# Optimization experiments

Hardware: AMD Instinct MI355X
Metric: run time of the kernel (lower is better)

Reference implementation:

```python
import jax, jax.numpy as jnp
import numpy as np

B, S, D, H = 4, 2048, 768, 12
HD = D // H  # head_dim = 64


def setup_inputs() -> dict:
    key = jax.random.key(0)
    ks = jax.random.split(key, 5)
    scale = 0.02
    return {
        "x": jax.random.normal(ks[0], (B, S, D), dtype=jnp.float32),
        "wq": jax.random.normal(ks[1], (D, D), dtype=jnp.float32) * scale,
        "wk": jax.random.normal(ks[2], (D, D), dtype=jnp.float32) * scale,
        "wv": jax.random.normal(ks[3], (D, D), dtype=jnp.float32) * scale,
        "wo": jax.random.normal(ks[4], (D, D), dtype=jnp.float32) * scale,
        "bo": jnp.zeros((D,), dtype=jnp.float32),
    }


def reference(x, wq, wk, wv, wo, bo):
    b, s, d = x.shape
    # torch Linear: y = x @ W.T ; qkv_bias=False
    q = (x @ wq.T).reshape(b, s, H, HD).transpose(0, 2, 1, 3)  # [b,h,s,hd]
    k = (x @ wk.T).reshape(b, s, H, HD).transpose(0, 2, 1, 3)
    v = (x @ wv.T).reshape(b, s, H, HD).transpose(0, 2, 1, 3)
    scores = jnp.einsum("bhqd,bhkd->bhqk", q, k)  # full [b,h,s,s] score matrix
    causal = jnp.triu(jnp.ones((s, s), dtype=bool), k=1)
    scores = jnp.where(causal, -jnp.inf, scores)
    attn = jax.nn.softmax(scores / jnp.sqrt(jnp.float32(HD)), axis=-1)
    ctx = jnp.einsum("bhqk,bhkd->bhqd", attn, v)
    ctx = ctx.transpose(0, 2, 1, 3).reshape(b, s, d)
    return ctx @ wo.T + bo  # dropout is identity in eval mode
```

## Files before the change

### kernel.cpp

```cpp
#include <hip/hip_runtime.h>

#define H 12
#define S 2048
#define D 768
#define HD 64
#define BATCH 4
#define M_TOT (BATCH * S)

typedef __attribute__((ext_vector_type(8))) short bf16x8;
typedef __attribute__((ext_vector_type(4))) float f32x4;

__device__ __forceinline__ ushort f2bf(float f) {
  unsigned int x = __float_as_uint(f);
  x += 0x7fffu + ((x >> 16) & 1u);
  return (ushort)(x >> 16);
}

__device__ __forceinline__ uint cvt_pk_bf16(float lo, float hi) {
  uint r;
  asm("v_cvt_pk_bf16_f32 %0, %1, %2" : "=v"(r) : "v"(lo), "v"(hi));
  return r;
}

__device__ __forceinline__ void gload_lds16(const void* gsrc, void* lds) {
  __builtin_amdgcn_global_load_lds(
      (const __attribute__((address_space(1))) unsigned int*)gsrc,
      (__attribute__((address_space(3))) unsigned int*)lds, 16, 0, 0);
}

__global__ __launch_bounds__(256) void cast_all(
    const float* __restrict__ x, const float* __restrict__ wq,
    const float* __restrict__ wk, const float* __restrict__ wv,
    const float* __restrict__ wo, ushort* __restrict__ xb,
    ushort* __restrict__ wqb, ushort* __restrict__ wkb,
    ushort* __restrict__ wvb, ushort* __restrict__ wob) {
  const int NX = M_TOT * D / 4;
  const int NW = D * D / 4;
  int i = blockIdx.x * 256 + threadIdx.x;
  const float* src; ushort* dst; int off;
  if (i < NX) { src = x; dst = xb; off = i; }
  else {
    int j = i - NX; int w = j / NW; off = j - w * NW;
    src = (w == 0) ? wq : (w == 1) ? wk : (w == 2) ? wv : wo;
    dst = (w == 0) ? wqb : (w == 1) ? wkb : (w == 2) ? wvb : wob;
  }
  float4 f = reinterpret_cast<const float4*>(src)[off];
  ushort4 u;
  u.x = f2bf(f.x); u.y = f2bf(f.y); u.z = f2bf(f.z); u.w = f2bf(f.w);
  reinterpret_cast<ushort4*>(dst)[off] = u;
}

__global__ __launch_bounds__(256) void gemm128(const ushort* __restrict__ A,
                                               const ushort* __restrict__ W0,
                                               const ushort* __restrict__ W1,
                                               ushort* __restrict__ o0,
                                               ushort* __restrict__ o1,
                                               float* __restrict__ out_f,
                                               const float* __restrict__ bias,
                                               int mode, float oscale) {
  __shared__ ushort SM[2][8192];
  const int tid = threadIdx.x;
  const int lane = tid & 63, wid = tid >> 6;
  const int g = lane >> 4, li = lane & 15;
  const int wm = wid >> 1, wn = wid & 1;
  const int m0 = blockIdx.x * 128;
  const ushort* Wp = W0;
  ushort* ob = o0;
  float osc = oscale;
  int n0;
  if (mode == 0) {
    int y = blockIdx.y;
    if (y >= 6) { Wp = W1; ob = o1; osc = 1.0f; }
    n0 = (y % 6) * 128;
  } else {
    n0 = blockIdx.y * 128;
  }

  const int rsub = lane >> 2;
  const int coff = (((lane & 3) ^ ((rsub >> 1) & 3)) << 3);

  auto stage = [&](int buf, int k0) {
#pragma unroll
    for (int rnd = 0; rnd < 2; ++rnd) {
      const int row0 = rnd * 64 + wid * 16;
      gload_lds16(&A[(size_t)(m0 + row0 + rsub) * 768 + k0 + coff], &SM[buf][row0 * 32]);
      gload_lds16(&Wp[(size_t)(n0 + row0 + rsub) * 768 + k0 + coff],
                  &SM[buf][4096 + row0 * 32]);
    }
  };

  f32x4 acc[4][4] = {};
  stage(0, 0);

  for (int kt = 0; kt < 24; ++kt) {
    const int cur = kt & 1;
    asm volatile("s_waitcnt vmcnt(0)" ::: "memory");
    __syncthreads();
    if (kt + 1 < 24) stage(cur ^ 1, (kt + 1) * 32);

    bf16x8 a[4], b[4];
#pragma unroll
    for (int i = 0; i < 4; ++i) {
      const int row = wm * 64 + i * 16 + li;
      a[i] = *reinterpret_cast<const bf16x8*>(
          &SM[cur][row * 32 + ((g ^ ((row >> 1) & 3)) << 3)]);
    }
#pragma unroll
    for (int j = 0; j < 4; ++j) {
      const int row = wn * 64 + j * 16 + li;
      b[j] = *reinterpret_cast<const bf16x8*>(
          &SM[cur][4096 + row * 32 + ((g ^ ((row >> 1) & 3)) << 3)]);
    }
    __builtin_amdgcn_s_setprio(1);
#pragma unroll
    for (int i = 0; i < 4; ++i)
#pragma unroll
      for (int j = 0; j < 4; ++j)
        acc[i][j] = __builtin_amdgcn_mfma_f32_16x16x32_bf16(a[i], b[j], acc[i][j], 0, 0, 0);
    __builtin_amdgcn_s_setprio(0);
  }

  if (mode == 1) {
#pragma unroll
    for (int i = 0; i < 4; ++i)
#pragma unroll
      for (int j = 0; j < 4; ++j)
#pragma unroll
        for (int r = 0; r < 4; ++r) {
          const int m = m0 + wm * 64 + i * 16 + g * 4 + r;
          const int n = n0 + wn * 64 + j * 16 + li;
          out_f[(size_t)m * 768 + n] = acc[i][j][r] + bias[n];
        }
    return;
  }

  __syncthreads();
  ushort* Cs = &SM[0][0];
#pragma unroll
  for (int i = 0; i < 4; ++i)
#pragma unroll
    for (int j = 0; j < 4; ++j)
#pragma unroll
      for (int r = 0; r < 4; ++r) {
        const int row = wm * 64 + i * 16 + g * 4 + r;
        const int col = wn * 64 + j * 16 + li;
        const int pc = ((((col >> 3) ^ (row & 7)) << 3) | (col & 7));
        Cs[row * 128 + pc] = f2bf(acc[i][j][r] * osc);
      }
  __syncthreads();

  const int row = tid >> 1, half = tid & 1;
  ushort* dst;
  if (mode == 0) {
    const int m = m0 + row;
    const int b_ = m >> 11, s_ = m & 2047;
    const int h_ = (n0 >> 6) + half;
    dst = &ob[(((size_t)b_ * H + h_) * S + s_) * HD];
  } else {
    const int mf = m0 + row;
    const int b_ = n0 >> 11;
    const int h_ = mf >> 6, hd_ = mf & 63;
    dst = &ob[(((size_t)b_ * H + h_) * HD + hd_) * S + (n0 & 2047) + half * 64];
  }
#pragma unroll
  for (int c8 = 0; c8 < 8; ++c8) {
    const int col = half * 64 + c8 * 8;
    const int chunk = (col >> 3) ^ (row & 7);
    bf16x8 vv = *reinterpret_cast<const bf16x8*>(&Cs[row * 128 + chunk * 8]);
    *reinterpret_cast<bf16x8*>(&dst[c8 * 8]) = vv;
  }
}

__global__ __launch_bounds__(256) void attn_kernel(const ushort* __restrict__ Q,
                                                   const ushort* __restrict__ K,
                                                   const ushort* __restrict__ VT,
                                                   ushort* __restrict__ ctx) {
  __shared__ ushort Ks[2][64 * 64];
  __shared__ ushort Vts[2][64 * 64];
  __shared__ ushort Ps[4][32][72];

  const int tid = threadIdx.x;
  const int lane = tid & 63, wid = tid >> 6;
  const int g = lane >> 4, li = lane & 15;

  const int wg = blockIdx.x;
  const int xcd = wg & 7, t = wg >> 3;
  const int bh = xcd + 8 * (t >> 4);
  const int p = t & 15;
  const int qL = 64 * (31 - p);
  const int qS = 64 * p;

  const size_t base = (size_t)bh * S * HD;
  const size_t vtbase = (size_t)bh * HD * S;

  bf16x8 aq[2][2];
#pragma unroll
  for (int f = 0; f < 2; ++f) {
    const size_t qr = base + (size_t)((f ? qS : qL) + wid * 16 + li) * HD;
#pragma unroll
    for (int c = 0; c < 2; ++c)
      aq[f][c] = *reinterpret_cast<const bf16x8*>(&Q[qr + c * 32 + g * 8]);
  }

  f32x4 acc[2][4] = {};
  float lpart[2] = {0.f, 0.f};

  const int nkt = 32 - p;

  const int rsub = lane >> 3;
  const int c8e = (((lane & 7) ^ rsub) << 3);

  auto stage = [&](int buf, int k0) {
#pragma unroll
    for (int rnd = 0; rnd < 2; ++rnd) {
      const int row0 = rnd * 32 + wid * 8;
      gload_lds16(&K[base + (size_t)(k0 + row0 + rsub) * HD + c8e], &Ks[buf][row0 << 6]);
      gload_lds16(&VT[vtbase + (size_t)(row0 + rsub) * S + k0 + c8e], &Vts[buf][row0 << 6]);
    }
  };

  stage(0, 0);

  for (int kt = 0; kt < nkt; ++kt) {
    const int cur = kt & 1;
    const int k0 = kt * 64;
    const bool doS = (kt <= p);

    asm volatile("s_waitcnt vmcnt(0)" ::: "memory");
    __syncthreads();
    if (kt + 1 < nkt) stage(cur ^ 1, k0 + 64);

    f32x4 sc[2][4];
    __builtin_amdgcn_s_setprio(1);
#pragma unroll
    for (int ct = 0; ct < 4; ++ct) {
      const int row = ct * 16 + li, r7 = row & 7;
      const ushort* kr = &Ks[cur][row << 6];
      bf16x8 kb0 = *reinterpret_cast<const bf16x8*>(&kr[(g ^ r7) << 3]);
      bf16x8 kb1 = *reinterpret_cast<const bf16x8*>(&kr[((4 + g) ^ r7) << 3]);
      {
        f32x4 z = {};
        z = __builtin_amdgcn_mfma_f32_16x16x32_bf16(kb0, aq[0][0], z, 0, 0, 0);
        z = __builtin_amdgcn_mfma_f32_16x16x32_bf16(kb1, aq[0][1], z, 0, 0, 0);
        sc[0][ct] = z;
      }
      if (doS) {
        f32x4 z = {};
        z = __builtin_amdgcn_mfma_f32_16x16x32_bf16(kb0, aq[1][0], z, 0, 0, 0);
        z = __builtin_amdgcn_mfma_f32_16x16x32_bf16(kb1, aq[1][1], z, 0, 0, 0);
        sc[1][ct] = z;
      }
    }
    __builtin_amdgcn_s_setprio(0);

    if (kt == nkt - 1) {
      const int q = qL + wid * 16 + li;
#pragma unroll
      for (int ct = 0; ct < 4; ++ct)
#pragma unroll
        for (int r = 0; r < 4; ++r)
          if (k0 + ct * 16 + 4 * g + r > q) sc[0][ct][r] = -1e30f;
    }
    if (kt == p) {
      const int q = qS + wid * 16 + li;
#pragma unroll
      for (int ct = 0; ct < 4; ++ct)
#pragma unroll
        for (int r = 0; r < 4; ++r)
          if (k0 + ct * 16 + 4 * g + r > q) sc[1][ct][r] = -1e30f;
    }

#pragma unroll
    for (int f = 0; f < 2; ++f) {
      if (f == 1 && !doS) break;
#pragma unroll
      for (int ct = 0; ct < 4; ++ct) {
        float p0 = __builtin_amdgcn_exp2f(sc[f][ct][0]);
        float p1 = __builtin_amdgcn_exp2f(sc[f][ct][1]);
        float p2 = __builtin_amdgcn_exp2f(sc[f][ct][2]);
        float p3 = __builtin_amdgcn_exp2f(sc[f][ct][3]);
        lpart[f] += (p0 + p1) + (p2 + p3);
        uint2 pw;
        pw.x = cvt_pk_bf16(p0, p1);
        pw.y = cvt_pk_bf16(p2, p3);
        *reinterpret_cast<uint2*>(&Ps[wid][f * 16 + li][ct * 16 + 4 * g]) = pw;
      }
    }

    bf16x8 pa[2][2];
    pa[0][0] = *reinterpret_cast<const bf16x8*>(&Ps[wid][li][g * 8]);
    pa[0][1] = *reinterpret_cast<const bf16x8*>(&Ps[wid][li][32 + g * 8]);
    if (doS) {
      pa[1][0] = *reinterpret_cast<const bf16x8*>(&Ps[wid][16 + li][g * 8]);
      pa[1][1] = *reinterpret_cast<const bf16x8*>(&Ps[wid][16 + li][32 + g * 8]);
    }
    __builtin_amdgcn_s_setprio(1);
#pragma unroll
    for (int dt = 0; dt < 4; ++dt) {
      const int row = dt * 16 + li, r7 = row & 7;
      const ushort* vr = &Vts[cur][row << 6];
      bf16x8 vb0 = *reinterpret_cast<const bf16x8*>(&vr[(g ^ r7) << 3]);
      bf16x8 vb1 = *reinterpret_cast<const bf16x8*>(&vr[((4 + g) ^ r7) << 3]);
      acc[0][dt] = __builtin_amdgcn_mfma_f32_16x16x32_bf16(pa[0][0], vb0, acc[0][dt], 0, 0, 0);
      acc[0][dt] = __builtin_amdgcn_mfma_f32_16x16x32_bf16(pa[0][1], vb1, acc[0][dt], 0, 0, 0);
      if (doS) {
        acc[1][dt] = __builtin_amdgcn_mfma_f32_16x16x32_bf16(pa[1][0], vb0, acc[1][dt], 0, 0, 0);
        acc[1][dt] = __builtin_amdgcn_mfma_f32_16x16x32_bf16(pa[1][1], vb1, acc[1][dt], 0, 0, 0);
      }
    }
    __builtin_amdgcn_s_setprio(0);
  }

  const int b = bh / H, h = bh % H;
#pragma unroll
  for (int f = 0; f < 2; ++f) {
    float l = lpart[f];
    l += __shfl_xor(l, 16);
    l += __shfl_xor(l, 32);
#pragma unroll
    for (int r = 0; r < 4; ++r) {
      float inv = 1.0f / __shfl(l, 4 * g + r);
      const int s = (f ? qS : qL) + wid * 16 + 4 * g + r;
#pragma unroll
      for (int dt = 0; dt < 4; ++dt)
        ctx[((size_t)(b * S + s)) * D + h * HD + dt * 16 + li] =
            f2bf(acc[f][dt][r] * inv);
    }
  }
}

extern "C" void kernel_launch(void* const* d_in, const int* in_sizes, int n_in,
                              void* d_out, int out_size, void* d_ws, size_t ws_size,
                              hipStream_t stream) {
  (void)in_sizes; (void)n_in; (void)out_size; (void)ws_size;
  const float* x  = (const float*)d_in[0];
  const float* wq = (const float*)d_in[1];
  const float* wk = (const float*)d_in[2];
  const float* wv = (const float*)d_in[3];
  const float* wo = (const float*)d_in[4];
  const float* bo = (const float*)d_in[5];
  float* out = (float*)d_out;

  const size_t xn = (size_t)M_TOT * D;
  const size_t wn = (size_t)D * D;

  ushort* p = (ushort*)d_ws;
  ushort* x_bf  = p; p += xn;
  ushort* wq_bf = p; p += wn;
  ushort* wk_bf = p; p += wn;
  ushort* wv_bf = p; p += wn;
  ushort* wo_bf = p; p += wn;
  ushort* q_bf  = p; p += xn;
  ushort* k_bf  = p; p += xn;
  ushort* vt_bf = p; p += xn;
  ushort* ctx_bf = x_bf;

  cast_all<<<8448, 256, 0, stream>>>(x, wq, wk, wv, wo,
                                     x_bf, wq_bf, wk_bf, wv_bf, wo_bf);

  const float QSCALE = 0.125f * 1.44269504f;
  gemm128<<<dim3(64, 12), 256, 0, stream>>>(x_bf, wq_bf, wk_bf, q_bf, k_bf,
                                            nullptr, nullptr, 0, QSCALE);
  gemm128<<<dim3(6, 64), 256, 0, stream>>>(wv_bf, x_bf, nullptr, vt_bf, nullptr,
                                           nullptr, nullptr, 2, 1.0f);

  attn_kernel<<<768, 256, 0, stream>>>(q_bf, k_bf, vt_bf, ctx_bf);

  gemm128<<<dim3(64, 6), 256, 0, stream>>>(ctx_bf, wo_bf, nullptr, nullptr, nullptr,
                                           out, bo, 1, 0.f);
}
```

Before: 136.7 us.

## Use 32x32 MFMA in attention with register-only P and merge QKV GEMM launches

The attention kernel switches from 16x16x32 to 32x32x16 MFMA tiles. Each wave now owns 32 query rows, either all long-range or all short-range, and the P matrix moves from accumulator to operand layout through v_permlane32_swap instead of a shared-memory round trip. The Q/K and V^T projection GEMMs are merged into one launch, and the Wo GEMM gets its own specialized kernel without mode branches. This removes LDS traffic and a kernel launch. In exchange, short-query waves sit idle through most K-tile iterations, which costs load balance inside each block.

```diff
diff --git a/kernel.cpp b/kernel.cpp
--- a/kernel.cpp
+++ b/kernel.cpp
@@ -9,6 +9,7 @@
 
 typedef __attribute__((ext_vector_type(8))) short bf16x8;
 typedef __attribute__((ext_vector_type(4))) float f32x4;
+typedef __attribute__((ext_vector_type(16))) float f32x16;
 
 __device__ __forceinline__ ushort f2bf(float f) {
   unsigned int x = __float_as_uint(f);
@@ -20,6 +21,10 @@
   uint r;
   asm("v_cvt_pk_bf16_f32 %0, %1, %2" : "=v"(r) : "v"(lo), "v"(hi));
   return r;
+}
+
+__device__ __forceinline__ void plane32swap(uint& a, uint& b) {
+  asm volatile("v_permlane32_swap_b32 %0, %1" : "+v"(a), "+v"(b));
 }
 
 __device__ __forceinline__ void gload_lds16(const void* gsrc, void* lds) {
@@ -50,30 +55,33 @@
   reinterpret_cast<ushort4*>(dst)[off] = u;
 }
 
-__global__ __launch_bounds__(256) void gemm128(const ushort* __restrict__ A,
-                                               const ushort* __restrict__ W0,
-                                               const ushort* __restrict__ W1,
-                                               ushort* __restrict__ o0,
-                                               ushort* __restrict__ o1,
-                                               float* __restrict__ out_f,
-                                               const float* __restrict__ bias,
-                                               int mode, float oscale) {
+__global__ __launch_bounds__(256) void gemm_qkv(
+    const ushort* __restrict__ xb, const ushort* __restrict__ wqb,
+    const ushort* __restrict__ wkb, const ushort* __restrict__ wvb,
+    ushort* __restrict__ qb, ushort* __restrict__ kb_,
+    ushort* __restrict__ vtb, float qscale) {
   __shared__ ushort SM[2][8192];
   const int tid = threadIdx.x;
   const int lane = tid & 63, wid = tid >> 6;
   const int g = lane >> 4, li = lane & 15;
   const int wm = wid >> 1, wn = wid & 1;
-  const int m0 = blockIdx.x * 128;
-  const ushort* Wp = W0;
-  ushort* ob = o0;
-  float osc = oscale;
-  int n0;
-  if (mode == 0) {
-    int y = blockIdx.y;
-    if (y >= 6) { Wp = W1; ob = o1; osc = 1.0f; }
+
+  const int wg = blockIdx.x;
+  const ushort *Ap, *Wp; ushort* ob; float osc; int m0, n0; bool vt;
+  if (wg < 768) {
+    vt = false;
+    m0 = (wg & 63) * 128;
+    const int y = wg >> 6;
     n0 = (y % 6) * 128;
+    Ap = xb;
+    if (y < 6) { Wp = wqb; ob = qb; osc = qscale; }
+    else       { Wp = wkb; ob = kb_; osc = 1.0f; }
   } else {
-    n0 = blockIdx.y * 128;
+    vt = true;
+    const int t2 = wg - 768;
+    m0 = (t2 % 6) * 128;
+    n0 = (t2 / 6) * 128;
+    Ap = wvb; Wp = xb; ob = vtb; osc = 1.0f;
   }
 
   const int rsub = lane >> 2;
@@ -83,7 +91,7 @@
 #pragma unroll
     for (int rnd = 0; rnd < 2; ++rnd) {
       const int row0 = rnd * 64 + wid * 16;
-      gload_lds16(&A[(size_t)(m0 + row0 + rsub) * 768 + k0 + coff], &SM[buf][row0 * 32]);
+      gload_lds16(&Ap[(size_t)(m0 + row0 + rsub) * 768 + k0 + coff], &SM[buf][row0 * 32]);
       gload_lds16(&Wp[(size_t)(n0 + row0 + rsub) * 768 + k0 + coff],
                   &SM[buf][4096 + row0 * 32]);
     }
@@ -120,20 +128,6 @@
     __builtin_amdgcn_s_setprio(0);
   }
 
-  if (mode == 1) {
-#pragma unroll
-    for (int i = 0; i < 4; ++i)
-#pragma unroll
-      for (int j = 0; j < 4; ++j)
-#pragma unroll
-        for (int r = 0; r < 4; ++r) {
-          const int m = m0 + wm * 64 + i * 16 + g * 4 + r;
-          const int n = n0 + wn * 64 + j * 16 + li;
-          out_f[(size_t)m * 768 + n] = acc[i][j][r] + bias[n];
-        }
-    return;
-  }
-
   __syncthreads();
   ushort* Cs = &SM[0][0];
 #pragma unroll
@@ -151,7 +145,7 @@
 
   const int row = tid >> 1, half = tid & 1;
   ushort* dst;
-  if (mode == 0) {
+  if (!vt) {
     const int m = m0 + row;
     const int b_ = m >> 11, s_ = m & 2047;
     const int h_ = (n0 >> 6) + half;
@@ -171,39 +165,106 @@
   }
 }
 
+__global__ __launch_bounds__(256) void gemm_wo(const ushort* __restrict__ A,
+                                               const ushort* __restrict__ W,
+                                               float* __restrict__ out_f,
+                                               const float* __restrict__ bias) {
+  __shared__ ushort SM[2][8192];
+  const int tid = threadIdx.x;
+  const int lane = tid & 63, wid = tid >> 6;
+  const int g = lane >> 4, li = lane & 15;
+  const int wm = wid >> 1, wn = wid & 1;
+  const int m0 = blockIdx.x * 128, n0 = blockIdx.y * 128;
+
+  const int rsub = lane >> 2;
+  const int coff = (((lane & 3) ^ ((rsub >> 1) & 3)) << 3);
+
+  auto stage = [&](int buf, int k0) {
+#pragma unroll
+    for (int rnd = 0; rnd < 2; ++rnd) {
+      const int row0 = rnd * 64 + wid * 16;
+      gload_lds16(&A[(size_t)(m0 + row0 + rsub) * 768 + k0 + coff], &SM[buf][row0 * 32]);
+      gload_lds16(&W[(size_t)(n0 + row0 + rsub) * 768 + k0 + coff],
+                  &SM[buf][4096 + row0 * 32]);
+    }
+  };
+
+  f32x4 acc[4][4] = {};
+  stage(0, 0);
+
+  for (int kt = 0; kt < 24; ++kt) {
+    const int cur = kt & 1;
+    asm volatile("s_waitcnt vmcnt(0)" ::: "memory");
+    __syncthreads();
+    if (kt + 1 < 24) stage(cur ^ 1, (kt + 1) * 32);
+
+    bf16x8 a[4], b[4];
+#pragma unroll
+    for (int i = 0; i < 4; ++i) {
+      const int row = wm * 64 + i * 16 + li;
+      a[i] = *reinterpret_cast<const bf16x8*>(
+          &SM[cur][row * 32 + ((g ^ ((row >> 1) & 3)) << 3)]);
+    }
+#pragma unroll
+    for (int j = 0; j < 4; ++j) {
+      const int row = wn * 64 + j * 16 + li;
+      b[j] = *reinterpret_cast<const bf16x8*>(
+          &SM[cur][4096 + row * 32 + ((g ^ ((row >> 1) & 3)) << 3)]);
+    }
+    __builtin_amdgcn_s_setprio(1);
+#pragma unroll
+    for (int i = 0; i < 4; ++i)
+#pragma unroll
+      for (int j = 0; j < 4; ++j)
+        acc[i][j] = __builtin_amdgcn_mfma_f32_16x16x32_bf16(a[i], b[j], acc[i][j], 0, 0, 0);
+    __builtin_amdgcn_s_setprio(0);
+  }
+
+#pragma unroll
+  for (int i = 0; i < 4; ++i)
+#pragma unroll
+    for (int j = 0; j < 4; ++j)
+#pragma unroll
+      for (int r = 0; r < 4; ++r) {
+        const int m = m0 + wm * 64 + i * 16 + g * 4 + r;
+        const int n = n0 + wn * 64 + j * 16 + li;
+        out_f[(size_t)m * 768 + n] = acc[i][j][r] + bias[n];
+      }
+}
+
 __global__ __launch_bounds__(256) void attn_kernel(const ushort* __restrict__ Q,
                                                    const ushort* __restrict__ K,
                                                    const ushort* __restrict__ VT,
                                                    ushort* __restrict__ ctx) {
   __shared__ ushort Ks[2][64 * 64];
   __shared__ ushort Vts[2][64 * 64];
-  __shared__ ushort Ps[4][32][72];
 
   const int tid = threadIdx.x;
   const int lane = tid & 63, wid = tid >> 6;
-  const int g = lane >> 4, li = lane & 15;
+  const int l31 = lane & 31, hi = lane >> 5;
 
   const int wg = blockIdx.x;
   const int xcd = wg & 7, t = wg >> 3;
   const int bh = xcd + 8 * (t >> 4);
   const int p = t & 15;
-  const int qL = 64 * (31 - p);
-  const int qS = 64 * p;
+  const int qL = 64 * (31 - p), qS = 64 * p;
+  const bool isLong = wid < 2;
+  const int q0w = isLong ? (qL + 32 * wid) : (qS + 32 * (wid - 2));
+  const int q = q0w + l31;
+  const int mytrips = isLong ? (32 - p) : (p + 1);
+  const int maskkt = isLong ? (31 - p) : p;
 
   const size_t base = (size_t)bh * S * HD;
   const size_t vtbase = (size_t)bh * HD * S;
 
-  bf16x8 aq[2][2];
-#pragma unroll
-  for (int f = 0; f < 2; ++f) {
-    const size_t qr = base + (size_t)((f ? qS : qL) + wid * 16 + li) * HD;
-#pragma unroll
-    for (int c = 0; c < 2; ++c)
-      aq[f][c] = *reinterpret_cast<const bf16x8*>(&Q[qr + c * 32 + g * 8]);
-  }
-
-  f32x4 acc[2][4] = {};
-  float lpart[2] = {0.f, 0.f};
+  bf16x8 qf[4];
+#pragma unroll
+  for (int ds_ = 0; ds_ < 4; ++ds_)
+    qf[ds_] = *reinterpret_cast<const bf16x8*>(
+        &Q[base + (size_t)q * HD + 16 * ds_ + 8 * hi]);
+
+  f32x16 acc[2] = {};
+  float lpart = 0.f;
 
   const int nkt = 32 - p;
 
@@ -224,109 +285,89 @@
   for (int kt = 0; kt < nkt; ++kt) {
     const int cur = kt & 1;
     const int k0 = kt * 64;
-    const bool doS = (kt <= p);
 
     asm volatile("s_waitcnt vmcnt(0)" ::: "memory");
     __syncthreads();
     if (kt + 1 < nkt) stage(cur ^ 1, k0 + 64);
-
-    f32x4 sc[2][4];
+    if (kt >= mytrips) continue;
+
+    f32x16 sc[2];
     __builtin_amdgcn_s_setprio(1);
 #pragma unroll
-    for (int ct = 0; ct < 4; ++ct) {
-      const int row = ct * 16 + li, r7 = row & 7;
+    for (int kb = 0; kb < 2; ++kb) {
+      const int row = 32 * kb + l31, r7 = row & 7;
       const ushort* kr = &Ks[cur][row << 6];
-      bf16x8 kb0 = *reinterpret_cast<const bf16x8*>(&kr[(g ^ r7) << 3]);
-      bf16x8 kb1 = *reinterpret_cast<const bf16x8*>(&kr[((4 + g) ^ r7) << 3]);
-      {
-        f32x4 z = {};
-        z = __builtin_amdgcn_mfma_f32_16x16x32_bf16(kb0, aq[0][0], z, 0, 0, 0);
-        z = __builtin_amdgcn_mfma_f32_16x16x32_bf16(kb1, aq[0][1], z, 0, 0, 0);
-        sc[0][ct] = z;
-      }
-      if (doS) {
-        f32x4 z = {};
-        z = __builtin_amdgcn_mfma_f32_16x16x32_bf16(kb0, aq[1][0], z, 0, 0, 0);
-        z = __builtin_amdgcn_mfma_f32_16x16x32_bf16(kb1, aq[1][1], z, 0, 0, 0);
-        sc[1][ct] = z;
-      }
+      f32x16 z = {};
+#pragma unroll
+      for (int ds_ = 0; ds_ < 4; ++ds_) {
+        bf16x8 ka = *reinterpret_cast<const bf16x8*>(&kr[((2 * ds_ + hi) ^ r7) << 3]);
+        z = __builtin_amdgcn_mfma_f32_32x32x16_bf16(ka, qf[ds_], z, 0, 0, 0);
+      }
+      sc[kb] = z;
     }
     __builtin_amdgcn_s_setprio(0);
 
-    if (kt == nkt - 1) {
-      const int q = qL + wid * 16 + li;
-#pragma unroll
-      for (int ct = 0; ct < 4; ++ct)
-#pragma unroll
-        for (int r = 0; r < 4; ++r)
-          if (k0 + ct * 16 + 4 * g + r > q) sc[0][ct][r] = -1e30f;
-    }
-    if (kt == p) {
-      const int q = qS + wid * 16 + li;
-#pragma unroll
-      for (int ct = 0; ct < 4; ++ct)
-#pragma unroll
-        for (int r = 0; r < 4; ++r)
-          if (k0 + ct * 16 + 4 * g + r > q) sc[1][ct][r] = -1e30f;
-    }
-
-#pragma unroll
-    for (int f = 0; f < 2; ++f) {
-      if (f == 1 && !doS) break;
-#pragma unroll
-      for (int ct = 0; ct < 4; ++ct) {
-        float p0 = __builtin_amdgcn_exp2f(sc[f][ct][0]);
-        float p1 = __builtin_amdgcn_exp2f(sc[f][ct][1]);
-        float p2 = __builtin_amdgcn_exp2f(sc[f][ct][2]);
-        float p3 = __builtin_amdgcn_exp2f(sc[f][ct][3]);
-        lpart[f] += (p0 + p1) + (p2 + p3);
-        uint2 pw;
-        pw.x = cvt_pk_bf16(p0, p1);
-        pw.y = cvt_pk_bf16(p2, p3);
-        *reinterpret_cast<uint2*>(&Ps[wid][f * 16 + li][ct * 16 + 4 * g]) = pw;
-      }
-    }
-
-    bf16x8 pa[2][2];
-    pa[0][0] = *reinterpret_cast<const bf16x8*>(&Ps[wid][li][g * 8]);
-    pa[0][1] = *reinterpret_cast<const bf16x8*>(&Ps[wid][li][32 + g * 8]);
-    if (doS) {
-      pa[1][0] = *reinterpret_cast<const bf16x8*>(&Ps[wid][16 + li][g * 8]);
-      pa[1][1] = *reinterpret_cast<const bf16x8*>(&Ps[wid][16 + li][32 + g * 8]);
-    }
+    if (kt == maskkt) {
+#pragma unroll
+      for (int kb = 0; kb < 2; ++kb) {
+        const int kbase = k0 + 32 * kb + 4 * hi;
+#pragma unroll
+        for (int r = 0; r < 16; ++r) {
+          const int k = kbase + (r & 3) + 8 * (r >> 2);
+          if (k > q) sc[kb][r] = -1e30f;
+        }
+      }
+    }
+
+    bf16x8 pf[4];
+#pragma unroll
+    for (int kb = 0; kb < 2; ++kb) {
+      float pv[16];
+#pragma unroll
+      for (int r = 0; r < 16; ++r) pv[r] = __builtin_amdgcn_exp2f(sc[kb][r]);
+#pragma unroll
+      for (int r = 0; r < 16; ++r) lpart += pv[r];
+#pragma unroll
+      for (int hf = 0; hf < 2; ++hf) {
+        uint a = cvt_pk_bf16(pv[8 * hf + 0], pv[8 * hf + 1]);
+        uint c = cvt_pk_bf16(pv[8 * hf + 2], pv[8 * hf + 3]);
+        uint b2 = cvt_pk_bf16(pv[8 * hf + 4], pv[8 * hf + 5]);
+        uint d2 = cvt_pk_bf16(pv[8 * hf + 6], pv[8 * hf + 7]);
+        plane32swap(a, b2);
+        plane32swap(c, d2);
+        uint4 u = {a, c, b2, d2};
+        pf[2 * kb + hf] = *reinterpret_cast<const bf16x8*>(&u);
+      }
+    }
+
     __builtin_amdgcn_s_setprio(1);
 #pragma unroll
-    for (int dt = 0; dt < 4; ++dt) {
-      const int row = dt * 16 + li, r7 = row & 7;
+    for (int db = 0; db < 2; ++db) {
+      const int row = 32 * db + l31, r7 = row & 7;
       const ushort* vr = &Vts[cur][row << 6];
-      bf16x8 vb0 = *reinterpret_cast<const bf16x8*>(&vr[(g ^ r7) << 3]);
-      bf16x8 vb1 = *reinterpret_cast<const bf16x8*>(&vr[((4 + g) ^ r7) << 3]);
-      acc[0][dt] = __builtin_amdgcn_mfma_f32_16x16x32_bf16(pa[0][0], vb0, acc[0][dt], 0, 0, 0);
-      acc[0][dt] = __builtin_amdgcn_mfma_f32_16x16x32_bf16(pa[0][1], vb1, acc[0][dt], 0, 0, 0);
-      if (doS) {
-        acc[1][dt] = __builtin_amdgcn_mfma_f32_16x16x32_bf16(pa[1][0], vb0, acc[1][dt], 0, 0, 0);
-        acc[1][dt] = __builtin_amdgcn_mfma_f32_16x16x32_bf16(pa[1][1], vb1, acc[1][dt], 0, 0, 0);
+#pragma unroll
+      for (int ks2 = 0; ks2 < 4; ++ks2) {
+        bf16x8 va = *reinterpret_cast<const bf16x8*>(&vr[((2 * ks2 + hi) ^ r7) << 3]);
+        acc[db] = __builtin_amdgcn_mfma_f32_32x32x16_bf16(va, pf[ks2], acc[db], 0, 0, 0);
       }
     }
     __builtin_amdgcn_s_setprio(0);
   }
 
+  float l = lpart;
+  l += __shfl_xor(l, 32);
+  const float inv = 1.0f / l;
   const int b = bh / H, h = bh % H;
-#pragma unroll
-  for (int f = 0; f < 2; ++f) {
-    float l = lpart[f];
-    l += __shfl_xor(l, 16);
-    l += __shfl_xor(l, 32);
-#pragma unroll
-    for (int r = 0; r < 4; ++r) {
-      float inv = 1.0f / __shfl(l, 4 * g + r);
-      const int s = (f ? qS : qL) + wid * 16 + 4 * g + r;
-#pragma unroll
-      for (int dt = 0; dt < 4; ++dt)
-        ctx[((size_t)(b * S + s)) * D + h * HD + dt * 16 + li] =
-            f2bf(acc[f][dt][r] * inv);
-    }
-  }
+  ushort* crow = &ctx[(size_t)(b * S + q) * D + h * HD];
+#pragma unroll
+  for (int db = 0; db < 2; ++db)
+#pragma unroll
+    for (int qd = 0; qd < 4; ++qd) {
+      uint2 pw;
+      pw.x = cvt_pk_bf16(acc[db][4 * qd + 0] * inv, acc[db][4 * qd + 1] * inv);
+      pw.y = cvt_pk_bf16(acc[db][4 * qd + 2] * inv, acc[db][4 * qd + 3] * inv);
+      *reinterpret_cast<uint2*>(&crow[32 * db + 8 * qd + 4 * hi]) = pw;
+    }
 }
 
 extern "C" void kernel_launch(void* const* d_in, const int* in_sizes, int n_in,
@@ -359,13 +400,10 @@
                                      x_bf, wq_bf, wk_bf, wv_bf, wo_bf);
 
   const float QSCALE = 0.125f * 1.44269504f;
-  gemm128<<<dim3(64, 12), 256, 0, stream>>>(x_bf, wq_bf, wk_bf, q_bf, k_bf,
-                                            nullptr, nullptr, 0, QSCALE);
-  gemm128<<<dim3(6, 64), 256, 0, stream>>>(wv_bf, x_bf, nullptr, vt_bf, nullptr,
-                                           nullptr, nullptr, 2, 1.0f);
+  gemm_qkv<<<1152, 256, 0, stream>>>(x_bf, wq_bf, wk_bf, wv_bf,
+                                     q_bf, k_bf, vt_bf, QSCALE);
 
   attn_kernel<<<768, 256, 0, stream>>>(q_bf, k_bf, vt_bf, ctx_bf);
 
-  gemm128<<<dim3(64, 6), 256, 0, stream>>>(ctx_bf, wo_bf, nullptr, nullptr, nullptr,
-                                           out, bo, 1, 0.f);
-}
+  gemm_wo<<<dim3(64, 6), 256, 0, stream>>>(ctx_bf, wo_bf, out, bo);
+}
```

New measurement: 153.3 us. 1.12x slower.
